# Kernel tuning notes

Hardware: AMD Instinct MI355X
Metric: run time of the kernel (lower is better)

Reference implementation:

```python
import jax, jax.numpy as jnp
import numpy as np

B, N, C, H = 4, 1024, 768, 12
D = C // H          # head_dim = 64
SCALE = D ** -0.5
EPS = 1e-5
LAMBDA_INIT = 0.8 - 0.6 * float(np.exp(-0.3 * (1 - 1)))  # layer_idx=1 -> 0.2


def _ln(x, w, b):
    mu = jnp.mean(x, axis=-1, keepdims=True)
    var = jnp.mean(jnp.square(x - mu), axis=-1, keepdims=True)
    return (x - mu) * jax.lax.rsqrt(var + EPS) * w + b


def setup_inputs() -> dict:
    key = jax.random.key(0)
    ks = jax.random.split(key, 16)
    s = lambda fan_in: 1.0 / np.sqrt(fan_in)
    return {
        "x": jax.random.normal(ks[0], (B, N, C), jnp.float32),
        "norm1_w": jnp.ones((C,), jnp.float32),
        "norm1_b": jnp.zeros((C,), jnp.float32),
        # torch Linear weights are [out, in]
        "wq": jax.random.normal(ks[1], (2 * C, C), jnp.float32) * s(C),
        "wk": jax.random.normal(ks[2], (2 * C, C), jnp.float32) * s(C),
        "wv": jax.random.normal(ks[3], (2 * C, C), jnp.float32) * s(C),
        "lambda_param": jnp.asarray(1.0, jnp.float32),
        "attn_ln_w": jnp.ones((2 * D,), jnp.float32),
        "attn_ln_b": jnp.zeros((2 * D,), jnp.float32),
        "proj_w": jax.random.normal(ks[4], (C, 2 * C), jnp.float32) * s(2 * C),
        "proj_b": jnp.zeros((C,), jnp.float32),
        "norm2_w": jnp.ones((C,), jnp.float32),
        "norm2_b": jnp.zeros((C,), jnp.float32),
        "fc1_w": jax.random.normal(ks[5], (4 * C, C), jnp.float32) * s(C),
        "fc1_b": jnp.zeros((4 * C,), jnp.float32),
        "fc2_w": jax.random.normal(ks[6], (C, 4 * C), jnp.float32) * s(4 * C),
        "fc2_b": jnp.zeros((C,), jnp.float32),
    }


def reference(x, norm1_w, norm1_b, wq, wk, wv, lambda_param, attn_ln_w, attn_ln_b,
              proj_w, proj_b, norm2_w, norm2_b, fc1_w, fc1_b, fc2_w, fc2_b):
    # --- pre-norm differential attention ---
    xn = _ln(x, norm1_w, norm1_b)                              # [B,N,C]
    def heads(w):  # project and split into heads: [B,H,N,2D]
        return (xn @ w.T).reshape(B, N, H, 2 * D).transpose(0, 2, 1, 3)
    q, k, v = heads(wq), heads(wk), heads(wv)
    q1, q2 = q[..., :D], q[..., D:]
    k1, k2 = k[..., :D], k[..., D:]
    attn1 = jax.nn.softmax(jnp.einsum('bhnd,bhmd->bhnm', q1, k1) * SCALE, axis=-1)
    attn2 = jax.nn.softmax(jnp.einsum('bhnd,bhmd->bhnm', q2, k2) * SCALE, axis=-1)
    diff = jnp.einsum('bhnm,bhmd->bhnd', attn1 - lambda_param * attn2, v)  # [B,H,N,2D]
    out = _ln(diff, attn_ln_w, attn_ln_b) * (1.0 - LAMBDA_INIT)
    out = out.transpose(0, 2, 1, 3).reshape(B, N, 2 * C)       # concat heads
    attn_out = out @ proj_w.T + proj_b                          # [B,N,C]
    x = x + attn_out
    # --- pre-norm MLP ---
    xn2 = _ln(x, norm2_w, norm2_b)
    h = jax.nn.gelu(xn2 @ fc1_w.T + fc1_b, approximate=False)
    x = x + (h @ fc2_w.T + fc2_b)
    return x
```

## Files before the change

### kernel.cpp

```cpp
#include <hip/hip_runtime.h>
#include <math.h>


typedef __bf16 bf16_t;
typedef __attribute__((ext_vector_type(8))) __bf16 bf16x8;
typedef __attribute__((ext_vector_type(4))) __bf16 bf16x4;
typedef __attribute__((ext_vector_type(4))) float  floatx4;

constexpr int Bb = 4, Nn = 1024, Cc = 768, Hh = 12;
constexpr int Rr = Bb * Nn;
constexpr float EPS_ = 1e-5f;
constexpr float QSCALE_ = 0.125f * 1.4426950408889634f;

__device__ __forceinline__ floatx4 mfma16(bf16x8 a, bf16x8 b, floatx4 c) {
  return __builtin_amdgcn_mfma_f32_16x16x32_bf16(a, b, c, 0, 0, 0);
}

__device__ __forceinline__ void async16(bf16_t* lds, const bf16_t* g) {
  __builtin_amdgcn_global_load_lds(
      (__attribute__((address_space(1))) void*)g,
      (__attribute__((address_space(3))) void*)lds, 16, 0, 0);
}

__global__ __launch_bounds__(256) void convert_weights(
    const float* __restrict__ s0, const float* __restrict__ s1,
    const float* __restrict__ s2, const float* __restrict__ s3,
    const float* __restrict__ s4, const float* __restrict__ s5,
    bf16_t* __restrict__ dst) {
  const size_t e = ((size_t)blockIdx.x * 256 + threadIdx.x) * 4;
  const float* src; size_t off; float sc = 1.0f;
  if      (e < 1179648u) { src = s0; off = e;            sc = QSCALE_; }
  else if (e < 2359296u) { src = s1; off = e - 1179648u; }
  else if (e < 3538944u) { src = s2; off = e - 2359296u; }
  else if (e < 4718592u) { src = s3; off = e - 3538944u; }
  else if (e < 7077888u) { src = s4; off = e - 4718592u; }
  else                   { src = s5; off = e - 7077888u; }
  const float4 f = *(const float4*)(src + off);
  bf16x4 o;
  o[0] = (__bf16)(f.x * sc); o[1] = (__bf16)(f.y * sc);
  o[2] = (__bf16)(f.z * sc); o[3] = (__bf16)(f.w * sc);
  *(bf16x4*)(dst + e) = o;
}

__global__ __launch_bounds__(256) void ln_kernel(
    const float* __restrict__ x, const float* __restrict__ w,
    const float* __restrict__ b, bf16_t* __restrict__ out) {
  const int row = blockIdx.x, t = threadIdx.x;
  const float* xr = x + (size_t)row * Cc;
  const float v0 = xr[t], v1 = xr[t + 256], v2 = xr[t + 512];
  float s  = v0 + v1 + v2;
  float s2 = v0 * v0 + v1 * v1 + v2 * v2;
#pragma unroll
  for (int off = 32; off > 0; off >>= 1) {
    s  += __shfl_down(s, off);
    s2 += __shfl_down(s2, off);
  }
  __shared__ float ws_[4], ws2_[4];
  if ((t & 63) == 0) { ws_[t >> 6] = s; ws2_[t >> 6] = s2; }
  __syncthreads();
  const float S  = ws_[0] + ws_[1] + ws_[2] + ws_[3];
  const float S2 = ws2_[0] + ws2_[1] + ws2_[2] + ws2_[3];
  const float mu  = S * (1.0f / Cc);
  const float inv = rsqrtf(S2 * (1.0f / Cc) - mu * mu + EPS_);
  bf16_t* orow = out + (size_t)row * Cc;
  orow[t]       = (bf16_t)((v0 - mu) * inv * w[t]       + b[t]);
  orow[t + 256] = (bf16_t)((v1 - mu) * inv * w[t + 256] + b[t + 256]);
  orow[t + 512] = (bf16_t)((v2 - mu) * inv * w[t + 512] + b[t + 512]);
}

template <int EPI>
__global__ __launch_bounds__(256, 3) void gemm_kernel(
    const bf16_t* __restrict__ A, const bf16_t* __restrict__ W,
    int K, int F,
    const float* __restrict__ bias, const float* __restrict__ resid,
    void* __restrict__ outp) {
  __shared__ alignas(16) bf16_t ldsA[128 * 32];
  __shared__ alignas(16) bf16_t ldsB[128 * 32];
  const int t = threadIdx.x, wave = t >> 6, lane = t & 63;
  const int quad = lane >> 4, l16 = lane & 15;
  const int wm = (wave & 1) * 64, wn = (wave >> 1) * 64;
  const int f0 = blockIdx.x * 128, r0 = blockIdx.y * 128;
  const int srow = lane >> 2, scol = (lane & 3) * 8;

  const bf16_t* ga0 = A + (size_t)(r0 + wave * 32 + srow) * K + scol;
  const bf16_t* ga1 = ga0 + (size_t)16 * K;
  const bf16_t* gb0 = W + (size_t)(f0 + wave * 32 + srow) * K + scol;
  const bf16_t* gb1 = gb0 + (size_t)16 * K;
  bf16_t* la0 = &ldsA[(wave * 2 + 0) * 512];
  bf16_t* la1 = &ldsA[(wave * 2 + 1) * 512];
  bf16_t* lb0 = &ldsB[(wave * 2 + 0) * 512];
  bf16_t* lb1 = &ldsB[(wave * 2 + 1) * 512];

  floatx4 acc[4][4] = {};

  for (int k0 = 0; k0 < K; k0 += 32) {
    __syncthreads();
    async16(la0, ga0 + k0);
    async16(la1, ga1 + k0);
    async16(lb0, gb0 + k0);
    async16(lb1, gb1 + k0);
    __syncthreads();

    bf16x8 af[4], bfr[4];
#pragma unroll
    for (int mt = 0; mt < 4; mt++)
      af[mt] = *(const bf16x8*)&ldsA[(wm + mt * 16 + l16) * 32 + quad * 8];
#pragma unroll
    for (int nt = 0; nt < 4; nt++)
      bfr[nt] = *(const bf16x8*)&ldsB[(wn + nt * 16 + l16) * 32 + quad * 8];
#pragma unroll
    for (int mt = 0; mt < 4; mt++)
#pragma unroll
      for (int nt = 0; nt < 4; nt++)
        acc[mt][nt] = mfma16(af[mt], bfr[nt], acc[mt][nt]);
  }

#pragma unroll
  for (int mt = 0; mt < 4; mt++) {
#pragma unroll
    for (int nt = 0; nt < 4; nt++) {
#pragma unroll
      for (int rg = 0; rg < 4; rg++) {
        const int r = r0 + wm + mt * 16 + quad * 4 + rg;
        const int f = f0 + wn + nt * 16 + l16;
        const float v = acc[mt][nt][rg];
        if constexpr (EPI == 0) {
          const int b = r >> 10, n = r & 1023;
          bf16_t* qkv = (bf16_t*)outp;
          if (f < 1536) {
            const int h = f >> 7, d = f & 127;
            qkv[(((size_t)(b * Hh + h)) * Nn + n) * 128 + d] = (bf16_t)v;
          } else if (f < 3072) {
            const int f2 = f - 1536, h = f2 >> 7, d = f2 & 127;
            (qkv + (size_t)Rr * 1536)
                [(((size_t)(b * Hh + h)) * Nn + n) * 128 + d] = (bf16_t)v;
          } else {
            const int f2 = f - 3072, h = f2 >> 7, d = f2 & 127;
            (qkv + (size_t)2 * Rr * 1536)
                [(((size_t)(b * Hh + h)) * 128 + d) * Nn + n] = (bf16_t)v;
          }
        } else if constexpr (EPI == 2) {
          ((float*)outp)[(size_t)r * F + f] =
              v + bias[f] + resid[(size_t)r * F + f];
        } else {
          const float z = v + bias[f];
          const float g = 0.5f * z * (1.0f + erff(z * 0.70710678118f));
          ((bf16_t*)outp)[(size_t)r * F + f] = (bf16_t)g;
        }
      }
    }
  }
}

__global__ __launch_bounds__(256, 2) void attn_kernel(
    const bf16_t* __restrict__ Q, const bf16_t* __restrict__ Kk,
    const bf16_t* __restrict__ Vt, const float* __restrict__ lam,
    const float* __restrict__ lnw, const float* __restrict__ lnb,
    bf16_t* __restrict__ outp) {
  const int qblk = blockIdx.x, bh = blockIdx.y;
  const bf16_t* qp = Q  + (size_t)bh * Nn * 128;
  const bf16_t* kp = Kk + (size_t)bh * Nn * 128;
  const bf16_t* vp = Vt + (size_t)bh * 128 * Nn;

  __shared__ alignas(16) bf16_t ldsK[64 * 128];
  __shared__ alignas(16) bf16_t ldsV[128 * 64];
  __shared__ alignas(16) bf16_t ldsP[4][2][2][16 * 72];

  const int t = threadIdx.x, wave = t >> 6, lane = t & 63;
  const int quad = lane >> 4, l16 = lane & 15;

  bf16x8 bq[2][4];
#pragma unroll
  for (int qg = 0; qg < 2; qg++) {
    const size_t qrow = qblk * 128 + wave * 32 + qg * 16 + l16;
#pragma unroll
    for (int c = 0; c < 4; c++)
      bq[qg][c] = *(const bf16x8*)(qp + qrow * 128 + c * 32 + quad * 8);
  }

  const int ksg = wave * 4;
  const int krl = lane >> 4, kslot = lane & 15;
  const int vrl = lane >> 3, vslot = lane & 7;

  floatx4 o1[2][8] = {}, o2[2][8] = {};
  float l1a[2] = {0.f, 0.f}, l2a[2] = {0.f, 0.f};

  for (int kt = 0; kt < 16; kt++) {
    __syncthreads();
#pragma unroll
    for (int j = 0; j < 4; j++) {
      const int seg = ksg + j;
      {
        const int r = seg * 4 + krl;
        const int cg = (kslot >> 2) ^ (r & 3), ci = kslot & 3;
        async16(&ldsK[seg * 512],
                kp + (size_t)(kt * 64 + r) * 128 + cg * 32 + ci * 8);
      }
      {
        const int r = seg * 8 + vrl;
        const int sg = vslot ^ (r & 7);
        async16(&ldsV[seg * 512], vp + (size_t)r * Nn + kt * 64 + sg * 8);
      }
    }
    __syncthreads();

#pragma unroll
    for (int ktile = 0; ktile < 4; ktile++) {
      bf16x8 ak[4];
#pragma unroll
      for (int c = 0; c < 4; c++)
        ak[c] = *(const bf16x8*)&ldsK[(ktile * 16 + l16) * 128 +
                                      ((c ^ (l16 & 3)) * 32) + quad * 8];
#pragma unroll
      for (int qg = 0; qg < 2; qg++) {
        floatx4 s1 = {}, s2 = {};
        s1 = mfma16(ak[0], bq[qg][0], s1);
        s1 = mfma16(ak[1], bq[qg][1], s1);
        s2 = mfma16(ak[2], bq[qg][2], s2);
        s2 = mfma16(ak[3], bq[qg][3], s2);
        bf16x4 p1, p2;
        float a1 = 0.f, a2 = 0.f;
#pragma unroll
        for (int rg = 0; rg < 4; rg++) {
          const float e1 = exp2f(s1[rg]);
          const float e2 = exp2f(s2[rg]);
          p1[rg] = (__bf16)e1; p2[rg] = (__bf16)e2;
          a1 += (float)p1[rg]; a2 += (float)p2[rg];
        }
        l1a[qg] += a1; l2a[qg] += a2;
        const int po = l16 * 72 + ktile * 16 + quad * 4;
        *(bf16x4*)&ldsP[wave][0][qg][po] = p1;
        *(bf16x4*)&ldsP[wave][1][qg][po] = p2;
      }
    }

    bf16x8 ap1[2][2], ap2[2][2];
#pragma unroll
    for (int qg = 0; qg < 2; qg++)
#pragma unroll
      for (int c = 0; c < 2; c++) {
        const int po = l16 * 72 + c * 32 + quad * 8;
        ap1[qg][c] = *(const bf16x8*)&ldsP[wave][0][qg][po];
        ap2[qg][c] = *(const bf16x8*)&ldsP[wave][1][qg][po];
      }
#pragma unroll
    for (int dt = 0; dt < 8; dt++) {
      const int r = dt * 16 + l16;
      bf16x8 bv[2];
#pragma unroll
      for (int c = 0; c < 2; c++)
        bv[c] = *(const bf16x8*)&ldsV[r * 64 + (((c * 4 + quad) ^ (r & 7)) * 8)];
#pragma unroll
      for (int qg = 0; qg < 2; qg++) {
        o1[qg][dt] = mfma16(ap1[qg][0], bv[0], o1[qg][dt]);
        o1[qg][dt] = mfma16(ap1[qg][1], bv[1], o1[qg][dt]);
        o2[qg][dt] = mfma16(ap2[qg][0], bv[0], o2[qg][dt]);
        o2[qg][dt] = mfma16(ap2[qg][1], bv[1], o2[qg][dt]);
      }
    }
  }

#pragma unroll
  for (int qg = 0; qg < 2; qg++) {
    l1a[qg] += __shfl_xor(l1a[qg], 16); l1a[qg] += __shfl_xor(l1a[qg], 32);
    l2a[qg] += __shfl_xor(l2a[qg], 16); l2a[qg] += __shfl_xor(l2a[qg], 32);
  }

  const float lambda = *lam;
  const int b = bh / Hh, h = bh % Hh;

#pragma unroll
  for (int qg = 0; qg < 2; qg++) {
    float inv1[4], inv2[4];
#pragma unroll
    for (int rg = 0; rg < 4; rg++) {
      const int qr = quad * 4 + rg;
      inv1[rg] = 1.0f / __shfl(l1a[qg], qr);
      inv2[rg] = lambda / __shfl(l2a[qg], qr);
    }
    float vals[8][4];
    float sum[4] = {0.f, 0.f, 0.f, 0.f}, ssq[4] = {0.f, 0.f, 0.f, 0.f};
#pragma unroll
    for (int dt = 0; dt < 8; dt++)
#pragma unroll
      for (int rg = 0; rg < 4; rg++) {
        const float v = o1[qg][dt][rg] * inv1[rg] - o2[qg][dt][rg] * inv2[rg];
        vals[dt][rg] = v;
        sum[rg] += v; ssq[rg] += v * v;
      }
#pragma unroll
    for (int m = 8; m >= 1; m >>= 1)
#pragma unroll
      for (int rg = 0; rg < 4; rg++) {
        sum[rg] += __shfl_xor(sum[rg], m);
        ssq[rg] += __shfl_xor(ssq[rg], m);
      }
#pragma unroll
    for (int rg = 0; rg < 4; rg++) {
      const float mu  = sum[rg] * (1.0f / 128.0f);
      const float inv = rsqrtf(ssq[rg] * (1.0f / 128.0f) - mu * mu + EPS_);
      const int n = qblk * 128 + wave * 32 + qg * 16 + quad * 4 + rg;
      bf16_t* orow = outp + ((size_t)(b * Nn + n)) * 1536 + h * 128;
#pragma unroll
      for (int dt = 0; dt < 8; dt++) {
        const int d = dt * 16 + l16;
        orow[d] = (bf16_t)(((vals[dt][rg] - mu) * inv * lnw[d] + lnb[d]) * 0.8f);
      }
    }
  }
}

extern "C" void kernel_launch(void* const* d_in, const int* in_sizes, int n_in,
                              void* d_out, int out_size, void* d_ws,
                              size_t ws_size, hipStream_t stream) {
  (void)in_sizes; (void)n_in; (void)out_size; (void)ws_size;
  const float* x     = (const float*)d_in[0];
  const float* n1w   = (const float*)d_in[1];
  const float* n1b   = (const float*)d_in[2];
  const float* wq    = (const float*)d_in[3];
  const float* wk    = (const float*)d_in[4];
  const float* wv    = (const float*)d_in[5];
  const float* lam   = (const float*)d_in[6];
  const float* alnw  = (const float*)d_in[7];
  const float* alnb  = (const float*)d_in[8];
  const float* projw = (const float*)d_in[9];
  const float* projb = (const float*)d_in[10];
  const float* n2w   = (const float*)d_in[11];
  const float* n2b   = (const float*)d_in[12];
  const float* fc1w  = (const float*)d_in[13];
  const float* fc1b  = (const float*)d_in[14];
  const float* fc2w  = (const float*)d_in[15];
  const float* fc2b  = (const float*)d_in[16];
  float* out = (float*)d_out;

  char* p = (char*)d_ws;
  bf16_t* xn    = (bf16_t*)p; p += (size_t)Rr * Cc * 2;
  bf16_t* wbuf  = (bf16_t*)p; p += (size_t)9437184 * 2;
  bf16_t* qkv   = (bf16_t*)p; p += (size_t)3 * Rr * 1536 * 2;
  bf16_t* attnb = (bf16_t*)p; p += (size_t)Rr * 1536 * 2;
  float*  xmid  = (float*)p;  p += (size_t)Rr * Cc * 4;
  bf16_t* xn2   = (bf16_t*)p; p += (size_t)Rr * Cc * 2;
  bf16_t* hb    = (bf16_t*)p; p += (size_t)Rr * 3072 * 2;

  bf16_t* wqkv_b = wbuf;
  bf16_t* wpj_b  = wbuf + 3538944;
  bf16_t* wf1_b  = wbuf + 4718592;
  bf16_t* wf2_b  = wbuf + 7077888;

  convert_weights<<<9216, 256, 0, stream>>>(wq, wk, wv, projw, fc1w, fc2w, wbuf);
  ln_kernel<<<Rr, 256, 0, stream>>>(x, n1w, n1b, xn);

  gemm_kernel<0><<<dim3(36, 32), 256, 0, stream>>>(xn, wqkv_b, 768, 4608,
                                                   nullptr, nullptr, qkv);

  const bf16_t* qb  = qkv;
  const bf16_t* kb  = qkv + (size_t)Rr * 1536;
  const bf16_t* vtb = qkv + (size_t)2 * Rr * 1536;
  attn_kernel<<<dim3(8, 48), 256, 0, stream>>>(qb, kb, vtb, lam, alnw, alnb,
                                               attnb);

  gemm_kernel<2><<<dim3(6, 32), 256, 0, stream>>>(attnb, wpj_b, 1536, 768,
                                                  projb, x, xmid);
  ln_kernel<<<Rr, 256, 0, stream>>>(xmid, n2w, n2b, xn2);
  gemm_kernel<3><<<dim3(24, 32), 256, 0, stream>>>(xn2, wf1_b, 768, 3072,
                                                   fc1b, nullptr, hb);
  gemm_kernel<2><<<dim3(6, 32), 256, 0, stream>>>(hb, wf2_b, 3072, 768,
                                                  fc2b, xmid, out);
}
```

Before: 414.6 us.

## Rework attention to register-resident P via bpermute and add 64-row GEMM

The attention kernel drops LDS staging for K, V and P. It reads K and V fragments straight from global memory and moves the probability tiles between lanes with ds_bpermute instead of a round trip through shared memory. Blocks become 128 threads covering 64 query rows, with bh on the fast grid axis to improve K/V cache reuse, so there are twice as many blocks. The two N=768 GEMMs (proj and fc2) use a new 64-row-tile kernel to double the block count and fill more CUs. The trade-off is more global/L2 traffic and uncoalesced fragment loads in attention, in exchange for no LDS barriers and higher parallelism.

```diff
diff --git a/kernel.cpp b/kernel.cpp
--- a/kernel.cpp
+++ b/kernel.cpp
@@ -5,6 +5,7 @@
 typedef __bf16 bf16_t;
 typedef __attribute__((ext_vector_type(8))) __bf16 bf16x8;
 typedef __attribute__((ext_vector_type(4))) __bf16 bf16x4;
+typedef __attribute__((ext_vector_type(2))) __bf16 bf16x2;
 typedef __attribute__((ext_vector_type(4))) float  floatx4;
 
 constexpr int Bb = 4, Nn = 1024, Cc = 768, Hh = 12;
@@ -20,6 +21,17 @@
   __builtin_amdgcn_global_load_lds(
       (__attribute__((address_space(1))) void*)g,
       (__attribute__((address_space(3))) void*)lds, 16, 0, 0);
+}
+
+__device__ __forceinline__ int pack2bf(float a, float b) {
+  bf16x2 v; v[0] = (__bf16)a; v[1] = (__bf16)b;
+  int r; __builtin_memcpy(&r, &v, 4); return r;
+}
+
+__device__ __forceinline__ bf16x8 as_frag(const int* p) {
+  union { int i[4]; bf16x8 v; } u;
+  u.i[0] = p[0]; u.i[1] = p[1]; u.i[2] = p[2]; u.i[3] = p[3];
+  return u.v;
 }
 
 __global__ __launch_bounds__(256) void convert_weights(
@@ -72,8 +84,7 @@
 __global__ __launch_bounds__(256, 3) void gemm_kernel(
     const bf16_t* __restrict__ A, const bf16_t* __restrict__ W,
     int K, int F,
-    const float* __restrict__ bias, const float* __restrict__ resid,
-    void* __restrict__ outp) {
+    const float* __restrict__ bias, void* __restrict__ outp) {
   __shared__ alignas(16) bf16_t ldsA[128 * 32];
   __shared__ alignas(16) bf16_t ldsB[128 * 32];
   const int t = threadIdx.x, wave = t >> 6, lane = t & 63;
@@ -139,9 +150,6 @@
             (qkv + (size_t)2 * Rr * 1536)
                 [(((size_t)(b * Hh + h)) * 128 + d) * Nn + n] = (bf16_t)v;
           }
-        } else if constexpr (EPI == 2) {
-          ((float*)outp)[(size_t)r * F + f] =
-              v + bias[f] + resid[(size_t)r * F + f];
         } else {
           const float z = v + bias[f];
           const float g = 0.5f * z * (1.0f + erff(z * 0.70710678118f));
@@ -152,110 +160,147 @@
   }
 }
 
-__global__ __launch_bounds__(256, 2) void attn_kernel(
+__global__ __launch_bounds__(256, 4) void gemm64_kernel(
+    const bf16_t* __restrict__ A, const bf16_t* __restrict__ W,
+    int K, int F,
+    const float* __restrict__ bias, const float* __restrict__ resid,
+    float* __restrict__ outp) {
+  __shared__ alignas(16) bf16_t ldsA[64 * 32];
+  __shared__ alignas(16) bf16_t ldsB[128 * 32];
+  const int t = threadIdx.x, wave = t >> 6, lane = t & 63;
+  const int quad = lane >> 4, l16 = lane & 15;
+  const int wm = (wave & 1) * 32, wn = (wave >> 1) * 64;
+  const int f0 = blockIdx.x * 128, r0 = blockIdx.y * 64;
+  const int srow = lane >> 2, scol = (lane & 3) * 8;
+
+  const bf16_t* ga = A + (size_t)(r0 + wave * 16 + srow) * K + scol;
+  const bf16_t* gb0 = W + (size_t)(f0 + wave * 32 + srow) * K + scol;
+  const bf16_t* gb1 = gb0 + (size_t)16 * K;
+  bf16_t* la  = &ldsA[wave * 512];
+  bf16_t* lb0 = &ldsB[(wave * 2 + 0) * 512];
+  bf16_t* lb1 = &ldsB[(wave * 2 + 1) * 512];
+
+  floatx4 acc[2][4] = {};
+
+  for (int k0 = 0; k0 < K; k0 += 32) {
+    __syncthreads();
+    async16(la, ga + k0);
+    async16(lb0, gb0 + k0);
+    async16(lb1, gb1 + k0);
+    __syncthreads();
+
+    bf16x8 af[2], bfr[4];
+#pragma unroll
+    for (int mt = 0; mt < 2; mt++)
+      af[mt] = *(const bf16x8*)&ldsA[(wm + mt * 16 + l16) * 32 + quad * 8];
+#pragma unroll
+    for (int nt = 0; nt < 4; nt++)
+      bfr[nt] = *(const bf16x8*)&ldsB[(wn + nt * 16 + l16) * 32 + quad * 8];
+#pragma unroll
+    for (int mt = 0; mt < 2; mt++)
+#pragma unroll
+      for (int nt = 0; nt < 4; nt++)
+        acc[mt][nt] = mfma16(af[mt], bfr[nt], acc[mt][nt]);
+  }
+
+#pragma unroll
+  for (int mt = 0; mt < 2; mt++)
+#pragma unroll
+    for (int nt = 0; nt < 4; nt++)
+#pragma unroll
+      for (int rg = 0; rg < 4; rg++) {
+        const int r = r0 + wm + mt * 16 + quad * 4 + rg;
+        const int f = f0 + wn + nt * 16 + l16;
+        outp[(size_t)r * F + f] =
+            acc[mt][nt][rg] + bias[f] + resid[(size_t)r * F + f];
+      }
+}
+
+__global__ __launch_bounds__(128, 2) void attn_kernel(
     const bf16_t* __restrict__ Q, const bf16_t* __restrict__ Kk,
     const bf16_t* __restrict__ Vt, const float* __restrict__ lam,
     const float* __restrict__ lnw, const float* __restrict__ lnb,
     bf16_t* __restrict__ outp) {
-  const int qblk = blockIdx.x, bh = blockIdx.y;
+  const int bh = blockIdx.x, qblk = blockIdx.y;
   const bf16_t* qp = Q  + (size_t)bh * Nn * 128;
   const bf16_t* kp = Kk + (size_t)bh * Nn * 128;
   const bf16_t* vp = Vt + (size_t)bh * 128 * Nn;
 
-  __shared__ alignas(16) bf16_t ldsK[64 * 128];
-  __shared__ alignas(16) bf16_t ldsV[128 * 64];
-  __shared__ alignas(16) bf16_t ldsP[4][2][2][16 * 72];
-
   const int t = threadIdx.x, wave = t >> 6, lane = t & 63;
   const int quad = lane >> 4, l16 = lane & 15;
 
   bf16x8 bq[2][4];
 #pragma unroll
   for (int qg = 0; qg < 2; qg++) {
-    const size_t qrow = qblk * 128 + wave * 32 + qg * 16 + l16;
+    const size_t qrow = qblk * 64 + wave * 32 + qg * 16 + l16;
 #pragma unroll
     for (int c = 0; c < 4; c++)
       bq[qg][c] = *(const bf16x8*)(qp + qrow * 128 + c * 32 + quad * 8);
   }
 
-  const int ksg = wave * 4;
-  const int krl = lane >> 4, kslot = lane & 15;
-  const int vrl = lane >> 3, vslot = lane & 7;
+  const int idxs[2] = {((((lane >> 4) & 1) * 2 + 0) * 16 + l16) * 4,
+                       ((((lane >> 4) & 1) * 2 + 1) * 16 + l16) * 4};
+  const bool hi_half = (lane & 32) != 0;
 
   floatx4 o1[2][8] = {}, o2[2][8] = {};
   float l1a[2] = {0.f, 0.f}, l2a[2] = {0.f, 0.f};
 
   for (int kt = 0; kt < 16; kt++) {
-    __syncthreads();
-#pragma unroll
-    for (int j = 0; j < 4; j++) {
-      const int seg = ksg + j;
-      {
-        const int r = seg * 4 + krl;
-        const int cg = (kslot >> 2) ^ (r & 3), ci = kslot & 3;
-        async16(&ldsK[seg * 512],
-                kp + (size_t)(kt * 64 + r) * 128 + cg * 32 + ci * 8);
-      }
-      {
-        const int r = seg * 8 + vrl;
-        const int sg = vslot ^ (r & 7);
-        async16(&ldsV[seg * 512], vp + (size_t)r * Nn + kt * 64 + sg * 8);
-      }
-    }
-    __syncthreads();
-
-#pragma unroll
-    for (int ktile = 0; ktile < 4; ktile++) {
-      bf16x8 ak[4];
-#pragma unroll
-      for (int c = 0; c < 4; c++)
-        ak[c] = *(const bf16x8*)&ldsK[(ktile * 16 + l16) * 128 +
-                                      ((c ^ (l16 & 3)) * 32) + quad * 8];
-#pragma unroll
-      for (int qg = 0; qg < 2; qg++) {
-        floatx4 s1 = {}, s2 = {};
-        s1 = mfma16(ak[0], bq[qg][0], s1);
-        s1 = mfma16(ak[1], bq[qg][1], s1);
-        s2 = mfma16(ak[2], bq[qg][2], s2);
-        s2 = mfma16(ak[3], bq[qg][3], s2);
-        bf16x4 p1, p2;
-        float a1 = 0.f, a2 = 0.f;
-#pragma unroll
-        for (int rg = 0; rg < 4; rg++) {
-          const float e1 = exp2f(s1[rg]);
-          const float e2 = exp2f(s2[rg]);
-          p1[rg] = (__bf16)e1; p2[rg] = (__bf16)e2;
-          a1 += (float)p1[rg]; a2 += (float)p2[rg];
+    const int kb = kt * 64;
+#pragma unroll
+    for (int c32 = 0; c32 < 2; c32++) {
+      int pk[2][2][2][2];
+#pragma unroll
+      for (int tt = 0; tt < 2; tt++) {
+        const int krow = kb + c32 * 32 + tt * 16 + l16;
+        bf16x8 ak[4];
+#pragma unroll
+        for (int c = 0; c < 4; c++)
+          ak[c] = *(const bf16x8*)(kp + (size_t)krow * 128 + c * 32 + quad * 8);
+#pragma unroll
+        for (int qg = 0; qg < 2; qg++) {
+          floatx4 s1 = {}, s2 = {};
+          s1 = mfma16(ak[0], bq[qg][0], s1);
+          s1 = mfma16(ak[1], bq[qg][1], s1);
+          s2 = mfma16(ak[2], bq[qg][2], s2);
+          s2 = mfma16(ak[3], bq[qg][3], s2);
+          float e[4], f[4];
+#pragma unroll
+          for (int rg = 0; rg < 4; rg++) {
+            e[rg] = __builtin_amdgcn_exp2f(s1[rg]);
+            f[rg] = __builtin_amdgcn_exp2f(s2[rg]);
+          }
+          l1a[qg] += (e[0] + e[1]) + (e[2] + e[3]);
+          l2a[qg] += (f[0] + f[1]) + (f[2] + f[3]);
+          pk[tt][qg][0][0] = pack2bf(e[0], e[1]);
+          pk[tt][qg][0][1] = pack2bf(e[2], e[3]);
+          pk[tt][qg][1][0] = pack2bf(f[0], f[1]);
+          pk[tt][qg][1][1] = pack2bf(f[2], f[3]);
         }
-        l1a[qg] += a1; l2a[qg] += a2;
-        const int po = l16 * 72 + ktile * 16 + quad * 4;
-        *(bf16x4*)&ldsP[wave][0][qg][po] = p1;
-        *(bf16x4*)&ldsP[wave][1][qg][po] = p2;
-      }
-    }
-
-    bf16x8 ap1[2][2], ap2[2][2];
-#pragma unroll
-    for (int qg = 0; qg < 2; qg++)
-#pragma unroll
-      for (int c = 0; c < 2; c++) {
-        const int po = l16 * 72 + c * 32 + quad * 8;
-        ap1[qg][c] = *(const bf16x8*)&ldsP[wave][0][qg][po];
-        ap2[qg][c] = *(const bf16x8*)&ldsP[wave][1][qg][po];
-      }
-#pragma unroll
-    for (int dt = 0; dt < 8; dt++) {
-      const int r = dt * 16 + l16;
-      bf16x8 bv[2];
-#pragma unroll
-      for (int c = 0; c < 2; c++)
-        bv[c] = *(const bf16x8*)&ldsV[r * 64 + (((c * 4 + quad) ^ (r & 7)) * 8)];
-#pragma unroll
-      for (int qg = 0; qg < 2; qg++) {
-        o1[qg][dt] = mfma16(ap1[qg][0], bv[0], o1[qg][dt]);
-        o1[qg][dt] = mfma16(ap1[qg][1], bv[1], o1[qg][dt]);
-        o2[qg][dt] = mfma16(ap2[qg][0], bv[0], o2[qg][dt]);
-        o2[qg][dt] = mfma16(ap2[qg][1], bv[1], o2[qg][dt]);
+      }
+      int aP[2][2][4];
+#pragma unroll
+      for (int qg = 0; qg < 2; qg++)
+#pragma unroll
+        for (int mat = 0; mat < 2; mat++)
+#pragma unroll
+          for (int i = 0; i < 4; i++) {
+            const int v0 = __builtin_amdgcn_ds_bpermute(idxs[i >> 1],
+                                                        pk[0][qg][mat][i & 1]);
+            const int v1 = __builtin_amdgcn_ds_bpermute(idxs[i >> 1],
+                                                        pk[1][qg][mat][i & 1]);
+            aP[qg][mat][i] = hi_half ? v1 : v0;
+          }
+      const bf16x8 a10 = as_frag(aP[0][0]), a11 = as_frag(aP[1][0]);
+      const bf16x8 a20 = as_frag(aP[0][1]), a21 = as_frag(aP[1][1]);
+#pragma unroll
+      for (int dt = 0; dt < 8; dt++) {
+        const bf16x8 bv = *(const bf16x8*)(vp + (size_t)(dt * 16 + l16) * Nn +
+                                           kb + c32 * 32 + quad * 8);
+        o1[0][dt] = mfma16(a10, bv, o1[0][dt]);
+        o1[1][dt] = mfma16(a11, bv, o1[1][dt]);
+        o2[0][dt] = mfma16(a20, bv, o2[0][dt]);
+        o2[1][dt] = mfma16(a21, bv, o2[1][dt]);
       }
     }
   }
@@ -299,7 +344,7 @@
     for (int rg = 0; rg < 4; rg++) {
       const float mu  = sum[rg] * (1.0f / 128.0f);
       const float inv = rsqrtf(ssq[rg] * (1.0f / 128.0f) - mu * mu + EPS_);
-      const int n = qblk * 128 + wave * 32 + qg * 16 + quad * 4 + rg;
+      const int n = qblk * 64 + wave * 32 + qg * 16 + quad * 4 + rg;
       bf16_t* orow = outp + ((size_t)(b * Nn + n)) * 1536 + h * 128;
 #pragma unroll
       for (int dt = 0; dt < 8; dt++) {
@@ -351,19 +396,19 @@
   ln_kernel<<<Rr, 256, 0, stream>>>(x, n1w, n1b, xn);
 
   gemm_kernel<0><<<dim3(36, 32), 256, 0, stream>>>(xn, wqkv_b, 768, 4608,
-                                                   nullptr, nullptr, qkv);
+                                                   nullptr, qkv);
 
   const bf16_t* qb  = qkv;
   const bf16_t* kb  = qkv + (size_t)Rr * 1536;
   const bf16_t* vtb = qkv + (size_t)2 * Rr * 1536;
-  attn_kernel<<<dim3(8, 48), 256, 0, stream>>>(qb, kb, vtb, lam, alnw, alnb,
-                                               attnb);
-
-  gemm_kernel<2><<<dim3(6, 32), 256, 0, stream>>>(attnb, wpj_b, 1536, 768,
-                                                  projb, x, xmid);
+  attn_kernel<<<dim3(48, 16), 128, 0, stream>>>(qb, kb, vtb, lam, alnw, alnb,
+                                                attnb);
+
+  gemm64_kernel<<<dim3(6, 64), 256, 0, stream>>>(attnb, wpj_b, 1536, 768,
+                                                 projb, x, xmid);
   ln_kernel<<<Rr, 256, 0, stream>>>(xmid, n2w, n2b, xn2);
   gemm_kernel<3><<<dim3(24, 32), 256, 0, stream>>>(xn2, wf1_b, 768, 3072,
-                                                   fc1b, nullptr, hb);
-  gemm_kernel<2><<<dim3(6, 32), 256, 0, stream>>>(hb, wf2_b, 3072, 768,
-                                                  fc2b, xmid, out);
-}
+                                                   fc1b, hb);
+  gemm64_kernel<<<dim3(6, 64), 256, 0, stream>>>(hb, wf2_b, 3072, 768,
+                                                 fc2b, xmid, out);
+}
```

Measured after the change: 502.5 us. 21.2% more time.

## Deepen GEMM K-tile to 64 and add 64-row GEMM for narrow outputs

Applied to the files above, without the earlier changes.

Doubles the K-step per LDS stage in the GEMM from 32 to 64, which halves the number of barrier pairs per K loop at the cost of twice the LDS per block. It also adds a separate 64x128-tile GEMM kernel for the two N=768 residual GEMMs (proj and fc2). That kernel launches 384 blocks instead of 192, so more of the CUs stay busy. The larger LDS footprint may limit occupancy, and the K-major LDS layout with row stride 64 may cause bank conflicts.

```diff
diff --git a/kernel.cpp b/kernel.cpp
--- a/kernel.cpp
+++ b/kernel.cpp
@@ -72,47 +72,48 @@
 __global__ __launch_bounds__(256, 3) void gemm_kernel(
     const bf16_t* __restrict__ A, const bf16_t* __restrict__ W,
     int K, int F,
-    const float* __restrict__ bias, const float* __restrict__ resid,
-    void* __restrict__ outp) {
-  __shared__ alignas(16) bf16_t ldsA[128 * 32];
-  __shared__ alignas(16) bf16_t ldsB[128 * 32];
+    const float* __restrict__ bias, void* __restrict__ outp) {
+  __shared__ alignas(16) bf16_t ldsA[128 * 64];
+  __shared__ alignas(16) bf16_t ldsB[128 * 64];
   const int t = threadIdx.x, wave = t >> 6, lane = t & 63;
   const int quad = lane >> 4, l16 = lane & 15;
   const int wm = (wave & 1) * 64, wn = (wave >> 1) * 64;
   const int f0 = blockIdx.x * 128, r0 = blockIdx.y * 128;
-  const int srow = lane >> 2, scol = (lane & 3) * 8;
-
-  const bf16_t* ga0 = A + (size_t)(r0 + wave * 32 + srow) * K + scol;
-  const bf16_t* ga1 = ga0 + (size_t)16 * K;
-  const bf16_t* gb0 = W + (size_t)(f0 + wave * 32 + srow) * K + scol;
-  const bf16_t* gb1 = gb0 + (size_t)16 * K;
-  bf16_t* la0 = &ldsA[(wave * 2 + 0) * 512];
-  bf16_t* la1 = &ldsA[(wave * 2 + 1) * 512];
-  bf16_t* lb0 = &ldsB[(wave * 2 + 0) * 512];
-  bf16_t* lb1 = &ldsB[(wave * 2 + 1) * 512];
+  const int srow = lane >> 3, scol = (lane & 7) * 8;
+
+  const bf16_t* ga = A + (size_t)(r0 + wave * 32 + srow) * K + scol;
+  const bf16_t* gb = W + (size_t)(f0 + wave * 32 + srow) * K + scol;
+  bf16_t* la = &ldsA[(wave * 32) * 64];
+  bf16_t* lb = &ldsB[(wave * 32) * 64];
 
   floatx4 acc[4][4] = {};
 
-  for (int k0 = 0; k0 < K; k0 += 32) {
-    __syncthreads();
-    async16(la0, ga0 + k0);
-    async16(la1, ga1 + k0);
-    async16(lb0, gb0 + k0);
-    async16(lb1, gb1 + k0);
-    __syncthreads();
-
-    bf16x8 af[4], bfr[4];
-#pragma unroll
-    for (int mt = 0; mt < 4; mt++)
-      af[mt] = *(const bf16x8*)&ldsA[(wm + mt * 16 + l16) * 32 + quad * 8];
-#pragma unroll
-    for (int nt = 0; nt < 4; nt++)
-      bfr[nt] = *(const bf16x8*)&ldsB[(wn + nt * 16 + l16) * 32 + quad * 8];
-#pragma unroll
-    for (int mt = 0; mt < 4; mt++)
+  for (int k0 = 0; k0 < K; k0 += 64) {
+    __syncthreads();
+#pragma unroll
+    for (int j = 0; j < 4; j++) {
+      async16(la + j * 512, ga + k0 + (size_t)(8 * j) * K);
+      async16(lb + j * 512, gb + k0 + (size_t)(8 * j) * K);
+    }
+    __syncthreads();
+
+#pragma unroll
+    for (int ks = 0; ks < 2; ks++) {
+      bf16x8 af[4], bfr[4];
+#pragma unroll
+      for (int mt = 0; mt < 4; mt++)
+        af[mt] =
+            *(const bf16x8*)&ldsA[(wm + mt * 16 + l16) * 64 + ks * 32 + quad * 8];
 #pragma unroll
       for (int nt = 0; nt < 4; nt++)
-        acc[mt][nt] = mfma16(af[mt], bfr[nt], acc[mt][nt]);
+        bfr[nt] =
+            *(const bf16x8*)&ldsB[(wn + nt * 16 + l16) * 64 + ks * 32 + quad * 8];
+#pragma unroll
+      for (int mt = 0; mt < 4; mt++)
+#pragma unroll
+        for (int nt = 0; nt < 4; nt++)
+          acc[mt][nt] = mfma16(af[mt], bfr[nt], acc[mt][nt]);
+    }
   }
 
 #pragma unroll
@@ -139,9 +140,6 @@
             (qkv + (size_t)2 * Rr * 1536)
                 [(((size_t)(b * Hh + h)) * 128 + d) * Nn + n] = (bf16_t)v;
           }
-        } else if constexpr (EPI == 2) {
-          ((float*)outp)[(size_t)r * F + f] =
-              v + bias[f] + resid[(size_t)r * F + f];
         } else {
           const float z = v + bias[f];
           const float g = 0.5f * z * (1.0f + erff(z * 0.70710678118f));
@@ -150,6 +148,68 @@
       }
     }
   }
+}
+
+__global__ __launch_bounds__(256, 4) void gemm64_kernel(
+    const bf16_t* __restrict__ A, const bf16_t* __restrict__ W,
+    int K, int F,
+    const float* __restrict__ bias, const float* __restrict__ resid,
+    float* __restrict__ outp) {
+  __shared__ alignas(16) bf16_t ldsA[64 * 64];
+  __shared__ alignas(16) bf16_t ldsB[128 * 64];
+  const int t = threadIdx.x, wave = t >> 6, lane = t & 63;
+  const int quad = lane >> 4, l16 = lane & 15;
+  const int wm = (wave & 1) * 32, wn = (wave >> 1) * 64;
+  const int f0 = blockIdx.x * 128, r0 = blockIdx.y * 64;
+  const int srow = lane >> 3, scol = (lane & 7) * 8;
+
+  const bf16_t* ga = A + (size_t)(r0 + wave * 16 + srow) * K + scol;
+  const bf16_t* gb = W + (size_t)(f0 + wave * 32 + srow) * K + scol;
+  bf16_t* la = &ldsA[(wave * 16) * 64];
+  bf16_t* lb = &ldsB[(wave * 32) * 64];
+
+  floatx4 acc[2][4] = {};
+
+  for (int k0 = 0; k0 < K; k0 += 64) {
+    __syncthreads();
+#pragma unroll
+    for (int j = 0; j < 2; j++)
+      async16(la + j * 512, ga + k0 + (size_t)(8 * j) * K);
+#pragma unroll
+    for (int j = 0; j < 4; j++)
+      async16(lb + j * 512, gb + k0 + (size_t)(8 * j) * K);
+    __syncthreads();
+
+#pragma unroll
+    for (int ks = 0; ks < 2; ks++) {
+      bf16x8 af[2], bfr[4];
+#pragma unroll
+      for (int mt = 0; mt < 2; mt++)
+        af[mt] =
+            *(const bf16x8*)&ldsA[(wm + mt * 16 + l16) * 64 + ks * 32 + quad * 8];
+#pragma unroll
+      for (int nt = 0; nt < 4; nt++)
+        bfr[nt] =
+            *(const bf16x8*)&ldsB[(wn + nt * 16 + l16) * 64 + ks * 32 + quad * 8];
+#pragma unroll
+      for (int mt = 0; mt < 2; mt++)
+#pragma unroll
+        for (int nt = 0; nt < 4; nt++)
+          acc[mt][nt] = mfma16(af[mt], bfr[nt], acc[mt][nt]);
+    }
+  }
+
+#pragma unroll
+  for (int mt = 0; mt < 2; mt++)
+#pragma unroll
+    for (int nt = 0; nt < 4; nt++)
+#pragma unroll
+      for (int rg = 0; rg < 4; rg++) {
+        const int r = r0 + wm + mt * 16 + quad * 4 + rg;
+        const int f = f0 + wn + nt * 16 + l16;
+        outp[(size_t)r * F + f] =
+            acc[mt][nt][rg] + bias[f] + resid[(size_t)r * F + f];
+      }
 }
 
 __global__ __launch_bounds__(256, 2) void attn_kernel(
@@ -351,7 +411,7 @@
   ln_kernel<<<Rr, 256, 0, stream>>>(x, n1w, n1b, xn);
 
   gemm_kernel<0><<<dim3(36, 32), 256, 0, stream>>>(xn, wqkv_b, 768, 4608,
-                                                   nullptr, nullptr, qkv);
+                                                   nullptr, qkv);
 
   const bf16_t* qb  = qkv;
   const bf16_t* kb  = qkv + (size_t)Rr * 1536;
@@ -359,11 +419,11 @@
   attn_kernel<<<dim3(8, 48), 256, 0, stream>>>(qb, kb, vtb, lam, alnw, alnb,
                                                attnb);
 
-  gemm_kernel<2><<<dim3(6, 32), 256, 0, stream>>>(attnb, wpj_b, 1536, 768,
-                                                  projb, x, xmid);
+  gemm64_kernel<<<dim3(6, 64), 256, 0, stream>>>(attnb, wpj_b, 1536, 768,
+                                                 projb, x, xmid);
   ln_kernel<<<Rr, 256, 0, stream>>>(xmid, n2w, n2b, xn2);
   gemm_kernel<3><<<dim3(24, 32), 256, 0, stream>>>(xn2, wf1_b, 768, 3072,
-                                                   fc1b, nullptr, hb);
-  gemm_kernel<2><<<dim3(6, 32), 256, 0, stream>>>(hb, wf2_b, 3072, 768,
-                                                  fc2b, xmid, out);
-}
+                                                   fc1b, hb);
+  gemm64_kernel<<<dim3(6, 64), 256, 0, stream>>>(hb, wf2_b, 3072, 768,
+                                                 fc2b, xmid, out);
+}
```

Measured after the change: 385.4 us. 7.0% less time.
